# Kernel tuning notes

Hardware: AMD Instinct MI355X
Metric: run time of the kernel (lower is better)

## Reference

```python
import jax, jax.numpy as jnp
import numpy as np

EPS = 1e-5  # BatchNorm1d default eps


def setup_inputs() -> dict:
    key = jax.random.key(0)
    k1, k2 = jax.random.split(key)
    b, d, h, w = 32, 256, 32, 128
    x = jax.random.normal(k1, (b, d, h, w), dtype=jnp.float32)
    # mask=True means padded/masked position (excluded from stats, left untouched)
    mask = jax.random.randint(k2, (b, 1, h, w), 0, 2).astype(bool)
    gamma = jnp.ones((d,), dtype=jnp.float32)
    beta = jnp.zeros((d,), dtype=jnp.float32)
    return {"x": x, "mask": mask, "gamma": gamma, "beta": beta}


def reference(x, mask, gamma, beta):
    # x: [b, d, h, w], mask: [b, 1, h, w] (True = masked)
    not_mask = ~mask[:, 0]                      # [b, h, w]
    wgt = not_mask.astype(x.dtype)              # [b, h, w]
    count = jnp.maximum(wgt.sum(), jnp.asarray(1.0, x.dtype))
    xt = jnp.transpose(x, (0, 2, 3, 1))         # [b, h, w, d]
    wm = wgt[..., None]                         # [b, h, w, 1]
    # masked per-channel batch statistics (biased variance, as BN training mode)
    mean = (xt * wm).sum(axis=(0, 1, 2)) / count                  # [d]
    var = (wm * (xt - mean) ** 2).sum(axis=(0, 1, 2)) / count     # [d]
    normed = (xt - mean) * jax.lax.rsqrt(var + EPS) * gamma + beta
    out = jnp.where(not_mask[..., None], normed, xt)              # scatter-back
    return jnp.transpose(out, (0, 3, 1, 2))     # [b, d, h, w]
```

## Files before the change

kernel.cpp:

```cpp
#include <hip/hip_runtime.h>

#define BB 32
#define DD 256
#define HW 4096
#define DHW (DD * HW)
#define TOTAL (BB * DHW)
#define EPS 1e-5f


__global__ void __launch_bounds__(256)
stats_kernel(const float* __restrict__ x, const int* __restrict__ mask,
             float* __restrict__ ws) {
    const int slice = blockIdx.x;
    const int b = slice >> 8;
    const int d = slice & 255;
    const float4* xs = reinterpret_cast<const float4*>(
        x + (size_t)b * DHW + (size_t)d * HW);
    const int4* ms = reinterpret_cast<const int4*>(mask + b * HW);
    const int tid = threadIdx.x;

    float sum = 0.f, sq = 0.f, cnt = 0.f;
#pragma unroll
    for (int j = 0; j < 4; ++j) {
        const int v = j * 256 + tid;
        float4 xv = xs[v];
        int4 mv = ms[v];
        if (!mv.x) { sum += xv.x; sq += xv.x * xv.x; cnt += 1.f; }
        if (!mv.y) { sum += xv.y; sq += xv.y * xv.y; cnt += 1.f; }
        if (!mv.z) { sum += xv.z; sq += xv.z * xv.z; cnt += 1.f; }
        if (!mv.w) { sum += xv.w; sq += xv.w * xv.w; cnt += 1.f; }
    }

#pragma unroll
    for (int off = 32; off > 0; off >>= 1) {
        sum += __shfl_down(sum, off);
        sq  += __shfl_down(sq, off);
        cnt += __shfl_down(cnt, off);
    }

    __shared__ float ssum[4], ssq[4], scnt[4];
    const int wave = tid >> 6, lane = tid & 63;
    if (lane == 0) { ssum[wave] = sum; ssq[wave] = sq; scnt[wave] = cnt; }
    __syncthreads();
    if (tid == 0) {
        float ts = 0.f, tq = 0.f, tc = 0.f;
#pragma unroll
        for (int i = 0; i < 4; ++i) { ts += ssum[i]; tq += ssq[i]; tc += scnt[i]; }
        atomicAdd(&ws[d], ts);
        atomicAdd(&ws[DD + d], tq);
        if (d == 0) atomicAdd(&ws[2 * DD], tc);
    }
}

__global__ void __launch_bounds__(256)
finalize_kernel(const float* __restrict__ gamma, const float* __restrict__ beta,
                float* __restrict__ ws) {
    const int d = threadIdx.x;
    const float count = fmaxf(ws[2 * DD], 1.0f);
    const float mean = ws[d] / count;
    float var = ws[DD + d] / count - mean * mean;
    var = fmaxf(var, 0.0f);
    const float scale = rsqrtf(var + EPS) * gamma[d];
    ws[2 * DD + 8 + d] = scale;
    ws[2 * DD + 8 + DD + d] = beta[d] - mean * scale;
}

__global__ void __launch_bounds__(256)
apply_kernel(const float* __restrict__ x, const int* __restrict__ mask,
             const float* __restrict__ ws, float* __restrict__ out) {
    const float* __restrict__ scale = ws + 2 * DD + 8;
    const float* __restrict__ bias  = ws + 2 * DD + 8 + DD;
    const int nvec = TOTAL / 4;
    const int stride = gridDim.x * blockDim.x;
    for (int v = blockIdx.x * blockDim.x + threadIdx.x; v < nvec; v += stride) {
        const int e = v << 2;
        const int b = e >> 20;
        const int rem = e & (DHW - 1);
        const int d = rem >> 12;
        const int pos = rem & 4095;
        float4 xv = reinterpret_cast<const float4*>(x)[v];
        int4 mv = reinterpret_cast<const int4*>(mask)[(b * HW + pos) >> 2];
        const float s = scale[d], bi = bias[d];
        float4 o;
        o.x = mv.x ? xv.x : xv.x * s + bi;
        o.y = mv.y ? xv.y : xv.y * s + bi;
        o.z = mv.z ? xv.z : xv.z * s + bi;
        o.w = mv.w ? xv.w : xv.w * s + bi;
        reinterpret_cast<float4*>(out)[v] = o;
    }
}

extern "C" void kernel_launch(void* const* d_in, const int* in_sizes, int n_in,
                              void* d_out, int out_size, void* d_ws, size_t ws_size,
                              hipStream_t stream) {
    const float* x     = (const float*)d_in[0];
    const int*   mask  = (const int*)d_in[1];
    const float* gamma = (const float*)d_in[2];
    const float* beta  = (const float*)d_in[3];
    float* out = (float*)d_out;
    float* ws  = (float*)d_ws;

    hipMemsetAsync(ws, 0, (2 * DD + 1) * sizeof(float), stream);

    stats_kernel<<<BB * DD, 256, 0, stream>>>(x, mask, ws);
    finalize_kernel<<<1, 256, 0, stream>>>(gamma, beta, ws);
    apply_kernel<<<2048, 256, 0, stream>>>(x, mask, ws, out);
}
```

Baseline: 80.43 us.

## Replace atomic stats with per-slice partials and fold finalize into apply

The stats kernel now writes a per-(batch, channel) partial sum and sum-of-squares plus a per-batch count instead of atomically accumulating into global counters. This removes the memset and the atomics. The separate finalize kernel is dropped, and every apply block reduces the 32 partials per channel into shared-memory scale and bias before its elementwise pass. That saves two launches and atomic contention, at the cost of each of the 2048 blocks redundantly reading about 16K floats of partials.

```diff
diff --git a/kernel.cpp b/kernel.cpp
--- a/kernel.cpp
+++ b/kernel.cpp
@@ -5,6 +5,7 @@
 #define HW 4096
 #define DHW (DD * HW)
 #define TOTAL (BB * DHW)
+#define NSLICE (BB * DD)
 #define EPS 1e-5f
 
 
@@ -46,33 +47,39 @@
         float ts = 0.f, tq = 0.f, tc = 0.f;
 #pragma unroll
         for (int i = 0; i < 4; ++i) { ts += ssum[i]; tq += ssq[i]; tc += scnt[i]; }
-        atomicAdd(&ws[d], ts);
-        atomicAdd(&ws[DD + d], tq);
-        if (d == 0) atomicAdd(&ws[2 * DD], tc);
+        ws[slice] = ts;
+        ws[NSLICE + slice] = tq;
+        if (d == 0) ws[2 * NSLICE + b] = tc;
     }
 }
 
 __global__ void __launch_bounds__(256)
-finalize_kernel(const float* __restrict__ gamma, const float* __restrict__ beta,
-                float* __restrict__ ws) {
-    const int d = threadIdx.x;
-    const float count = fmaxf(ws[2 * DD], 1.0f);
-    const float mean = ws[d] / count;
-    float var = ws[DD + d] / count - mean * mean;
-    var = fmaxf(var, 0.0f);
-    const float scale = rsqrtf(var + EPS) * gamma[d];
-    ws[2 * DD + 8 + d] = scale;
-    ws[2 * DD + 8 + DD + d] = beta[d] - mean * scale;
-}
+apply_kernel(const float* __restrict__ x, const int* __restrict__ mask,
+             const float* __restrict__ ws, const float* __restrict__ gamma,
+             const float* __restrict__ beta, float* __restrict__ out) {
+    __shared__ float s_scale[DD], s_bias[DD];
+    const int tid = threadIdx.x;
 
-__global__ void __launch_bounds__(256)
-apply_kernel(const float* __restrict__ x, const int* __restrict__ mask,
-             const float* __restrict__ ws, float* __restrict__ out) {
-    const float* __restrict__ scale = ws + 2 * DD + 8;
-    const float* __restrict__ bias  = ws + 2 * DD + 8 + DD;
+    float cnt = 0.f;
+#pragma unroll
+    for (int b = 0; b < BB; ++b) cnt += ws[2 * NSLICE + b];
+    cnt = fmaxf(cnt, 1.0f);
+    float sum = 0.f, sq = 0.f;
+#pragma unroll
+    for (int b = 0; b < BB; ++b) {
+        sum += ws[b * DD + tid];
+        sq  += ws[NSLICE + b * DD + tid];
+    }
+    const float mean = sum / cnt;
+    const float var = fmaxf(sq / cnt - mean * mean, 0.0f);
+    const float sc = rsqrtf(var + EPS) * gamma[tid];
+    s_scale[tid] = sc;
+    s_bias[tid] = beta[tid] - mean * sc;
+    __syncthreads();
+
     const int nvec = TOTAL / 4;
     const int stride = gridDim.x * blockDim.x;
-    for (int v = blockIdx.x * blockDim.x + threadIdx.x; v < nvec; v += stride) {
+    for (int v = blockIdx.x * blockDim.x + tid; v < nvec; v += stride) {
         const int e = v << 2;
         const int b = e >> 20;
         const int rem = e & (DHW - 1);
@@ -80,7 +87,7 @@
         const int pos = rem & 4095;
         float4 xv = reinterpret_cast<const float4*>(x)[v];
         int4 mv = reinterpret_cast<const int4*>(mask)[(b * HW + pos) >> 2];
-        const float s = scale[d], bi = bias[d];
+        const float s = s_scale[d], bi = s_bias[d];
         float4 o;
         o.x = mv.x ? xv.x : xv.x * s + bi;
         o.y = mv.y ? xv.y : xv.y * s + bi;
@@ -100,9 +107,6 @@
     float* out = (float*)d_out;
     float* ws  = (float*)d_ws;
 
-    hipMemsetAsync(ws, 0, (2 * DD + 1) * sizeof(float), stream);
-
-    stats_kernel<<<BB * DD, 256, 0, stream>>>(x, mask, ws);
-    finalize_kernel<<<1, 256, 0, stream>>>(gamma, beta, ws);
-    apply_kernel<<<2048, 256, 0, stream>>>(x, mask, ws, out);
+    stats_kernel<<<NSLICE, 256, 0, stream>>>(x, mask, ws);
+    apply_kernel<<<2048, 256, 0, stream>>>(x, mask, ws, gamma, beta, out);
 }
```

New measurement: 70.63 us. 1.14x faster.
